# Kernel optimization log

Measured on AMD Instinct MI355X. Metric: run time of the kernel, lower is better.

Reference implementation:

```python
import jax, jax.numpy as jnp
import numpy as np

DIM = 2048
INTER = 1408          # moe_inter_dim per routed expert
N_EXPERTS = 32
TOPK = 6
N_GROUPS = 8
TOPK_GROUPS = 4
ROUTE_SCALE = 2.5
SHARED_INTER = 2816   # n_shared_experts(2) * moe_inter_dim
T = 8192              # tokens (batch*seq flattened)
INIT = 0.02


def setup_inputs() -> dict:
    key = jax.random.key(0)
    k = jax.random.split(key, 8)
    x = jax.random.normal(k[0], (T, DIM), jnp.float32)
    gate_w = jax.random.normal(k[1], (N_EXPERTS, DIM), jnp.float32) * INIT
    # stacked routed-expert weights (torch Linear convention: [out, in])
    w1 = jax.random.normal(k[2], (N_EXPERTS, INTER, DIM), jnp.float32) * INIT
    w2 = jax.random.normal(k[3], (N_EXPERTS, DIM, INTER), jnp.float32) * INIT
    w3 = jax.random.normal(k[4], (N_EXPERTS, INTER, DIM), jnp.float32) * INIT
    # shared experts (single fused MLP, inter = n_shared * moe_inter_dim)
    sw1 = jax.random.normal(k[5], (SHARED_INTER, DIM), jnp.float32) * INIT
    sw2 = jax.random.normal(k[6], (DIM, SHARED_INTER), jnp.float32) * INIT
    sw3 = jax.random.normal(k[7], (SHARED_INTER, DIM), jnp.float32) * INIT
    return {"x": x, "gate_w": gate_w, "w1": w1, "w2": w2, "w3": w3,
            "sw1": sw1, "sw2": sw2, "sw3": sw3}


def _gate(x, gate_w):
    # sigmoid scores, no bias (dim != 7168), group-limited top-k routing
    scores = jax.nn.sigmoid(x @ gate_w.T)                  # (T, E)
    original = scores
    sg = scores.reshape(x.shape[0], N_GROUPS, -1)          # (T, G, E/G)
    group_scores = sg.max(axis=-1)                         # (T, G)  (amax branch)
    _, gidx = jax.lax.top_k(group_scores, TOPK_GROUPS)     # (T, Gk)
    gmask = jnp.zeros((x.shape[0], N_GROUPS), bool).at[
        jnp.arange(x.shape[0])[:, None], gidx].set(True)
    masked = jnp.where(gmask[:, :, None], sg, 0.0).reshape(x.shape[0], -1)
    _, idx = jax.lax.top_k(masked, TOPK)                   # (T, K)
    w = jnp.take_along_axis(original, idx, axis=1)         # gather pre-mask scores
    w = w / w.sum(axis=-1, keepdims=True)                  # sigmoid normalization
    w = w * ROUTE_SCALE
    return w.astype(x.dtype), idx


def reference(x, gate_w, w1, w2, w3, sw1, sw2, sw3):
    weights, idx = _gate(x, gate_w)                        # (T,K), (T,K) int
    # per-token combine weight for each expert: cw[t,e] = sum_k w[t,k]*[idx==e]
    onehot = jax.nn.one_hot(idx, N_EXPERTS, dtype=weights.dtype)  # (T,K,E)
    cw = jnp.einsum('tk,tke->et', weights, onehot)         # (E, T)

    def expert_step(acc, ew):
        W1, W2, W3, cwe = ew                               # cwe: (T,)
        h = jax.nn.silu(x @ W1.T) * (x @ W3.T)             # (T, INTER)
        return acc + cwe[:, None] * (h @ W2.T), None

    y, _ = jax.lax.scan(expert_step, jnp.zeros_like(x), (w1, w2, w3, cw))
    # shared experts MLP (SwiGLU)
    z = (jax.nn.silu(x @ sw1.T) * (x @ sw3.T)) @ sw2.T
    return y + z
```

## Files before the change

### kernel.cpp

```cpp
#include <hip/hip_runtime.h>
#include <hip/hip_bf16.h>
#include <stdint.h>

typedef unsigned short u16;

#define T_TOK 8192
#define DIM 2048
#define INTER 1408
#define NEXP 32
#define TOPK 6
#define SHINTER 2816
#define SLOTS (T_TOK * TOPK)

typedef __attribute__((ext_vector_type(8))) short bf16x8;
typedef __attribute__((ext_vector_type(4))) float f32x4;

__device__ inline u16 f2bf(float f) {
  union { float f; unsigned u; } c; c.f = f;
  unsigned r = (c.u + 0x7FFFu + ((c.u >> 16) & 1u)) >> 16;
  return (u16)r;
}
__device__ inline float bf2f(u16 h) {
  union { unsigned u; float f; } c; c.u = ((unsigned)h) << 16;
  return c.f;
}

__device__ __forceinline__ void gl16(const void* g, void* l) {
  __builtin_amdgcn_global_load_lds(
      (const __attribute__((address_space(1))) void*)g,
      (__attribute__((address_space(3))) void*)l, 16, 0, 0);
}

__global__ __launch_bounds__(256)
void gate_route_k(const float* __restrict__ x, const float* __restrict__ gw,
                  int* __restrict__ tidx, float* __restrict__ tw,
                  int* __restrict__ counts, u16* __restrict__ xb)
{
  int lane = threadIdx.x & 63, w = threadIdx.x >> 6;
  int t = blockIdx.x * 4 + w;
  __shared__ float sc[4][32];
  __shared__ float gm[4][8];
  const float* xr = x + (size_t)t * DIM + lane * 4;
  float4 xv[8];
#pragma unroll
  for (int i = 0; i < 8; i++) xv[i] = *(const float4*)(xr + i * 256);
  u16* xrow = xb + (size_t)t * DIM + lane * 4;
#pragma unroll
  for (int i = 0; i < 8; i++) {
    union { u16 h[4]; uint2 q; } p;
    p.h[0] = f2bf(xv[i].x); p.h[1] = f2bf(xv[i].y);
    p.h[2] = f2bf(xv[i].z); p.h[3] = f2bf(xv[i].w);
    *(uint2*)(xrow + i * 256) = p.q;
  }
  for (int e = 0; e < NEXP; e++) {
    const float* g = gw + (size_t)e * DIM + lane * 4;
    float acc = 0.f;
#pragma unroll
    for (int i = 0; i < 8; i++) {
      float4 gv = *(const float4*)(g + i * 256);
      acc += xv[i].x * gv.x + xv[i].y * gv.y + xv[i].z * gv.z + xv[i].w * gv.w;
    }
#pragma unroll
    for (int off = 32; off > 0; off >>= 1) acc += __shfl_down(acc, off);
    if (lane == 0) sc[w][e] = 1.f / (1.f + __expf(-acc));
  }
  if (lane == 0) {
#pragma unroll
    for (int g = 0; g < 8; g++)
      gm[w][g] = fmaxf(fmaxf(sc[w][g*4+0], sc[w][g*4+1]), fmaxf(sc[w][g*4+2], sc[w][g*4+3]));
    unsigned gsel = 0u;
    for (int it = 0; it < 4; it++) {
      float best = -1.f; int bi = 0;
      for (int g = 0; g < 8; g++)
        if (!((gsel >> g) & 1u) && gm[w][g] > best) { best = gm[w][g]; bi = g; }
      gsel |= 1u << bi;
    }
    unsigned chosen = 0u; float wsum = 0.f;
    int ids[TOPK]; float wv[TOPK];
#pragma unroll
    for (int it = 0; it < TOPK; it++) {
      float best = -1.f; int bi = 0;
      for (int e = 0; e < NEXP; e++)
        if (((gsel >> (e >> 2)) & 1u) && !((chosen >> e) & 1u) && sc[w][e] > best) { best = sc[w][e]; bi = e; }
      chosen |= 1u << bi; ids[it] = bi; wv[it] = best; wsum += best;
    }
    float s = 2.5f / wsum;
#pragma unroll
    for (int k = 0; k < TOPK; k++) {
      tidx[t * TOPK + k] = ids[k];
      tw[t * TOPK + k] = wv[k] * s;
      atomicAdd(&counts[ids[k]], 1);
    }
  }
}

__global__ void zero32(int* p) { if (threadIdx.x < NEXP) p[threadIdx.x] = 0; }

__global__ __launch_bounds__(1024)
void perm_build_k(const int* __restrict__ counts,
                  const int* __restrict__ tidx, const float* __restrict__ tw,
                  int* __restrict__ ptok, float* __restrict__ pw,
                  int* __restrict__ slotof,
                  int4* __restrict__ desc128, int* __restrict__ ntiles)
{
  int e = blockIdx.x;
  int tid = threadIdx.x, lane = tid & 63, w = tid >> 6;
  __shared__ int wsum[16];
  __shared__ int cursor;
  if (w == 0) {
    int c = (lane < NEXP) ? counts[lane] : 0;
    int inc = c;
#pragma unroll
    for (int d = 1; d < 64; d <<= 1) {
      int v = __shfl_up(inc, d);
      if (lane >= d) inc += v;
    }
    int off_e = inc - c;
    if (e == 0) {
      int nt = (c + 127) >> 7;
      int tinc = nt;
#pragma unroll
      for (int d = 1; d < 64; d <<= 1) {
        int v = __shfl_up(tinc, d);
        if (lane >= d) tinc += v;
      }
      int tex = tinc - nt;
      if (lane < NEXP) {
        for (int i = 0; i < nt; i++) {
          int rem = c - i * 128;
          desc128[tex + i] = make_int4(lane, off_e + i * 128, rem < 128 ? rem : 128, 0);
        }
      }
      if (lane == NEXP - 1) ntiles[0] = tinc;
    }
    if (lane == e) cursor = off_e;
  }
  __syncthreads();
  for (int start = 0; start < SLOTS; start += 1024) {
    int i = start + tid;
    int match = (tidx[i] == e) ? 1 : 0;
    unsigned long long b = __ballot(match);
    if (lane == 0) wsum[w] = __popcll(b);
    __syncthreads();
    int base = cursor;
    int waveoff = 0;
    for (int ww = 0; ww < w; ww++) waveoff += wsum[ww];
    int total = 0;
#pragma unroll
    for (int ww = 0; ww < 16; ww++) total += wsum[ww];
    if (match) {
      int before = __popcll(b & ((1ull << lane) - 1ull));
      int slot = base + waveoff + before;
      ptok[slot] = i / TOPK;
      pw[slot] = tw[i];
      slotof[i] = slot;
    }
    __syncthreads();
    if (tid == 0) cursor = base + total;
  }
}

__global__ __launch_bounds__(256)
void cvt3_k(const float* __restrict__ s0, const float* __restrict__ s1,
            const float* __restrict__ s2, u16* __restrict__ d0,
            u16* __restrict__ d1, u16* __restrict__ d2, int n8)
{
  const float* src = (blockIdx.y == 0) ? s0 : (blockIdx.y == 1) ? s1 : s2;
  u16*         dst = (blockIdx.y == 0) ? d0 : (blockIdx.y == 1) ? d1 : d2;
  int stride = gridDim.x * 256;
  for (size_t i = (size_t)blockIdx.x * 256 + threadIdx.x; i < (size_t)n8; i += stride) {
    size_t j = i * 8;
    float4 a = *(const float4*)(src + j);
    float4 b = *(const float4*)(src + j + 4);
    union { u16 h[8]; uint4 u; } p;
    p.h[0] = f2bf(a.x); p.h[1] = f2bf(a.y); p.h[2] = f2bf(a.z); p.h[3] = f2bf(a.w);
    p.h[4] = f2bf(b.x); p.h[5] = f2bf(b.y); p.h[6] = f2bf(b.z); p.h[7] = f2bf(b.w);
    *(uint4*)(dst + j) = p.u;
  }
}


#define UP_RSEG (416 * 11)
#define DN_SSEG (64 * 8)

__global__ __launch_bounds__(256, 2)
void up2m_k(const u16* __restrict__ xb,
            const u16* __restrict__ w1b, const u16* __restrict__ w3b,
            const u16* __restrict__ sw1b, const u16* __restrict__ sw3b,
            const int* __restrict__ ptok,
            const int4* __restrict__ desc, const int* __restrict__ ntiles,
            u16* __restrict__ H, u16* __restrict__ Hs)
{
  int bid = blockIdx.x;
  bool routed = bid < UP_RSEG;
  int slot_base, rows, n0, hld;
  const u16 *B1, *B3;
  u16* out;
  bool gather;
  if (routed) {
    int rt0 = bid % 416, ct = bid / 416;
    int rt = (rt0 & 7) * 52 + (rt0 >> 3);
    if (rt >= ntiles[0]) return;
    int4 d = desc[rt];
    slot_base = d.y; rows = d.z;
    size_t off = (size_t)d.x * (size_t)INTER * DIM;
    B1 = w1b + off; B3 = w3b + off;
    n0 = ct * 128; hld = INTER; out = H; gather = true;
  } else {
    int b2 = bid - UP_RSEG;
    int rt0 = b2 & 63, ct = b2 >> 6;
    int rt = (rt0 & 7) * 8 + (rt0 >> 3);
    slot_base = rt * 128; rows = 128;
    B1 = sw1b; B3 = sw3b;
    n0 = ct * 128; hld = SHINTER; out = Hs; gather = false;
  }
  int tid = threadIdx.x, lane = tid & 63;
  int w = tid >> 6, wr = w >> 1, wc = w & 1;

  __shared__ u16 As[128][64];
  __shared__ u16 Bs1[128][64];
  __shared__ u16 Bs3[128][64];

  int selem = (((lane & 7) ^ (lane >> 3)) * 8);
  const u16 *a_src[4], *b1_src[4], *b3_src[4];
#pragma unroll
  for (int s = 0; s < 4; s++) {
    int r = w * 32 + s * 8 + (lane >> 3);
    int tok;
    if (gather) { int rr = r < rows ? r : rows - 1; tok = ptok[slot_base + rr]; }
    else tok = slot_base + r;
    a_src[s]  = xb + (size_t)tok * DIM + selem;
    b1_src[s] = B1 + (size_t)(n0 + r) * DIM + selem;
    b3_src[s] = B3 + (size_t)(n0 + r) * DIM + selem;
  }

  f32x4 acc1[4][4], acc3[4][4];
#pragma unroll
  for (int m = 0; m < 4; m++)
#pragma unroll
    for (int n = 0; n < 4; n++) { acc1[m][n] = {0.f,0.f,0.f,0.f}; acc3[m][n] = {0.f,0.f,0.f,0.f}; }

  for (int kk = 0; kk < DIM / 64; kk++) {
    __syncthreads();
#pragma unroll
    for (int s = 0; s < 4; s++) {
      gl16(a_src[s]  + kk * 64, &As [w * 32 + s * 8][0]);
      gl16(b1_src[s] + kk * 64, &Bs1[w * 32 + s * 8][0]);
      gl16(b3_src[s] + kk * 64, &Bs3[w * 32 + s * 8][0]);
    }
    __syncthreads();
#pragma unroll
    for (int h = 0; h < 2; h++) {
      bf16x8 af[4], b1f[4], b3f[4];
      int chk = (h * 4 + (lane >> 4)) ^ (lane & 7);
#pragma unroll
      for (int m = 0; m < 4; m++)
        af[m] = *(const bf16x8*)&As[wr * 64 + m * 16 + (lane & 15)][chk * 8];
#pragma unroll
      for (int n = 0; n < 4; n++) {
        b1f[n] = *(const bf16x8*)&Bs1[wc * 64 + n * 16 + (lane & 15)][chk * 8];
        b3f[n] = *(const bf16x8*)&Bs3[wc * 64 + n * 16 + (lane & 15)][chk * 8];
      }
#pragma unroll
      for (int m = 0; m < 4; m++)
#pragma unroll
        for (int n = 0; n < 4; n++) {
          acc1[m][n] = __builtin_amdgcn_mfma_f32_16x16x32_bf16(af[m], b1f[n], acc1[m][n], 0, 0, 0);
          acc3[m][n] = __builtin_amdgcn_mfma_f32_16x16x32_bf16(af[m], b3f[n], acc3[m][n], 0, 0, 0);
        }
    }
  }
#pragma unroll
  for (int m = 0; m < 4; m++) {
#pragma unroll
    for (int r = 0; r < 4; r++) {
      int row_local = wr * 64 + m * 16 + (lane >> 4) * 4 + r;
      if (row_local < rows) {
        size_t rowp = (size_t)(slot_base + row_local) * hld + n0 + wc * 64 + (lane & 15);
#pragma unroll
        for (int n = 0; n < 4; n++) {
          float c1 = acc1[m][n][r], c3 = acc3[m][n][r];
          float hval = (c1 / (1.f + __expf(-c1))) * c3;
          out[rowp + n * 16] = f2bf(hval);
        }
      }
    }
  }
}

template<int KD, bool ROUTED>
__device__ __forceinline__ void down3_body(
    u16 (*As)[64], u16 (*Bs1)[64], u16 (*Bs2)[64],
    const u16* __restrict__ A0, const u16* __restrict__ B,
    int slot_base, int rows, int n0,
    const float* __restrict__ pw,
    u16* __restrict__ slotout, float* __restrict__ yout)
{
  constexpr int KSTEPS = KD / 64;
  int tid = threadIdx.x, lane = tid & 63;
  int w = tid >> 6, wr = w >> 1, wc = w & 1;

  int selem = (((lane & 7) ^ (lane >> 3)) * 8);
  const u16 *a_src[4], *b1_src[4], *b2_src[4];
#pragma unroll
  for (int s = 0; s < 4; s++) {
    int r = w * 32 + s * 8 + (lane >> 3);
    a_src[s]  = A0 + (size_t)(slot_base + r) * KD + selem;
    b1_src[s] = B + (size_t)(n0 + r) * KD + selem;
    b2_src[s] = B + (size_t)(n0 + 128 + r) * KD + selem;
  }

  f32x4 acc[4][8];
#pragma unroll
  for (int m = 0; m < 4; m++)
#pragma unroll
    for (int n = 0; n < 8; n++) acc[m][n] = {0.f, 0.f, 0.f, 0.f};

  for (int kk = 0; kk < KSTEPS; kk++) {
    __syncthreads();
#pragma unroll
    for (int s = 0; s < 4; s++) {
      gl16(a_src[s]  + kk * 64, &As [w * 32 + s * 8][0]);
      gl16(b1_src[s] + kk * 64, &Bs1[w * 32 + s * 8][0]);
      gl16(b2_src[s] + kk * 64, &Bs2[w * 32 + s * 8][0]);
    }
    __syncthreads();
#pragma unroll
    for (int h = 0; h < 2; h++) {
      bf16x8 af[4], bv1[4], bv2[4];
      int chk = (h * 4 + (lane >> 4)) ^ (lane & 7);
#pragma unroll
      for (int m = 0; m < 4; m++)
        af[m] = *(const bf16x8*)&As[wr * 64 + m * 16 + (lane & 15)][chk * 8];
#pragma unroll
      for (int n = 0; n < 4; n++) {
        bv1[n] = *(const bf16x8*)&Bs1[wc * 64 + n * 16 + (lane & 15)][chk * 8];
        bv2[n] = *(const bf16x8*)&Bs2[wc * 64 + n * 16 + (lane & 15)][chk * 8];
      }
#pragma unroll
      for (int m = 0; m < 4; m++)
#pragma unroll
        for (int n = 0; n < 4; n++) {
          acc[m][n]     = __builtin_amdgcn_mfma_f32_16x16x32_bf16(af[m], bv1[n], acc[m][n],     0, 0, 0);
          acc[m][n + 4] = __builtin_amdgcn_mfma_f32_16x16x32_bf16(af[m], bv2[n], acc[m][n + 4], 0, 0, 0);
        }
    }
  }
#pragma unroll
  for (int m = 0; m < 4; m++) {
#pragma unroll
    for (int r = 0; r < 4; r++) {
      int row_local = wr * 64 + m * 16 + (lane >> 4) * 4 + r;
      if (row_local < rows) {
        int slot = slot_base + row_local;
        size_t rp = (size_t)slot * DIM + n0 + wc * 64 + (lane & 15);
        if constexpr (ROUTED) {
          float sw = pw[slot];
#pragma unroll
          for (int n = 0; n < 4; n++) {
            slotout[rp + n * 16]       = f2bf(acc[m][n][r] * sw);
            slotout[rp + 128 + n * 16] = f2bf(acc[m][n + 4][r] * sw);
          }
        } else {
#pragma unroll
          for (int n = 0; n < 4; n++) {
            yout[rp + n * 16]       = acc[m][n][r];
            yout[rp + 128 + n * 16] = acc[m][n + 4][r];
          }
        }
      }
    }
  }
}

__global__ __launch_bounds__(256, 2)
void down3m_k(const u16* __restrict__ H, const u16* __restrict__ Hs,
              const u16* __restrict__ w2b, const u16* __restrict__ sw2b,
              const int4* __restrict__ desc, const int* __restrict__ ntiles,
              const float* __restrict__ pw,
              u16* __restrict__ slotout, float* __restrict__ yout)
{
  __shared__ u16 As[128][64];
  __shared__ u16 Bs1[128][64];
  __shared__ u16 Bs2[128][64];
  int bid = blockIdx.x;
  if (bid >= DN_SSEG) {
    int b2 = bid - DN_SSEG;
    int rt0 = b2 % 416, ct = b2 / 416;
    int rt = (rt0 & 7) * 52 + (rt0 >> 3);
    if (rt >= ntiles[0]) return;
    int4 d = desc[rt];
    down3_body<INTER, true>(As, Bs1, Bs2, H, w2b + (size_t)d.x * DIM * INTER,
                            d.y, d.z, ct * 256, pw, slotout, yout);
  } else {
    int rt0 = bid & 63, ct = bid >> 6;
    int rt = (rt0 & 7) * 8 + (rt0 >> 3);
    down3_body<SHINTER, false>(As, Bs1, Bs2, Hs, sw2b, rt * 128, 128, ct * 256,
                               pw, slotout, yout);
  }
}

template<bool SHARED>
__global__ __launch_bounds__(256, 2)
void up_gemm_k(const u16* __restrict__ xb,
               const float* __restrict__ W1g, const float* __restrict__ W3g,
               const int* __restrict__ ptok,
               const int4* __restrict__ desc, const int* __restrict__ ntiles,
               u16* __restrict__ Hout)
{
  constexpr int HLD = SHARED ? SHINTER : INTER;
  int row_tile = blockIdx.x, col_tile = blockIdx.y;
  int slot_base, rows;
  const float *B1, *B3;
  if constexpr (SHARED) {
    slot_base = row_tile * 128; rows = 128; B1 = W1g; B3 = W3g;
  } else {
    if (row_tile >= ntiles[0]) return;
    int4 d = desc[row_tile];
    slot_base = d.y; rows = d.z;
    size_t off = (size_t)d.x * (size_t)INTER * DIM;
    B1 = W1g + off; B3 = W3g + off;
  }
  int n0 = col_tile * 128;
  int tid = threadIdx.x, lane = tid & 63;
  int wv = tid >> 6, wr = wv >> 1, wc = wv & 1;

  __shared__ u16 As[128][72];
  __shared__ u16 Bs1[128][72];
  __shared__ u16 Bs3[128][72];

  int ar = tid >> 3, ac = (tid & 7) * 8;
  const u16* asrc[4];
#pragma unroll
  for (int s = 0; s < 4; s++) {
    int r = s * 32 + ar;
    int tok;
    if constexpr (SHARED) tok = slot_base + r;
    else { int rr = r < rows ? r : rows - 1; tok = ptok[slot_base + rr]; }
    asrc[s] = xb + (size_t)tok * DIM + ac;
  }
  int br = tid >> 4, bc = (tid & 15) * 4;
  const float* b1p = B1 + (size_t)(n0 + br) * DIM + bc;
  const float* b3p = B3 + (size_t)(n0 + br) * DIM + bc;

  f32x4 acc1[4][4], acc3[4][4];
#pragma unroll
  for (int m = 0; m < 4; m++)
#pragma unroll
    for (int n = 0; n < 4; n++) { acc1[m][n] = {0.f,0.f,0.f,0.f}; acc3[m][n] = {0.f,0.f,0.f,0.f}; }

  for (int kk = 0; kk < DIM / 64; kk++) {
    __syncthreads();
#pragma unroll
    for (int s = 0; s < 4; s++) {
      uint4 v = *(const uint4*)(asrc[s] + kk * 64);
      *(uint4*)&As[s * 32 + ar][ac] = v;
    }
#pragma unroll
    for (int s = 0; s < 8; s++) {
      float4 v = *(const float4*)(b1p + (size_t)(s * 16) * DIM + kk * 64);
      union { u16 h[4]; uint2 q; } o;
      o.h[0] = f2bf(v.x); o.h[1] = f2bf(v.y); o.h[2] = f2bf(v.z); o.h[3] = f2bf(v.w);
      *(uint2*)&Bs1[s * 16 + br][bc] = o.q;
    }
#pragma unroll
    for (int s = 0; s < 8; s++) {
      float4 v = *(const float4*)(b3p + (size_t)(s * 16) * DIM + kk * 64);
      union { u16 h[4]; uint2 q; } o;
      o.h[0] = f2bf(v.x); o.h[1] = f2bf(v.y); o.h[2] = f2bf(v.z); o.h[3] = f2bf(v.w);
      *(uint2*)&Bs3[s * 16 + br][bc] = o.q;
    }
    __syncthreads();
#pragma unroll
    for (int h = 0; h < 2; h++) {
      bf16x8 af[4], b1f[4], b3f[4];
#pragma unroll
      for (int m = 0; m < 4; m++)
        af[m] = *(const bf16x8*)&As[wr * 64 + m * 16 + (lane & 15)][h * 32 + (lane >> 4) * 8];
#pragma unroll
      for (int n = 0; n < 4; n++) {
        b1f[n] = *(const bf16x8*)&Bs1[wc * 64 + n * 16 + (lane & 15)][h * 32 + (lane >> 4) * 8];
        b3f[n] = *(const bf16x8*)&Bs3[wc * 64 + n * 16 + (lane & 15)][h * 32 + (lane >> 4) * 8];
      }
#pragma unroll
      for (int m = 0; m < 4; m++)
#pragma unroll
        for (int n = 0; n < 4; n++) {
          acc1[m][n] = __builtin_amdgcn_mfma_f32_16x16x32_bf16(af[m], b1f[n], acc1[m][n], 0, 0, 0);
          acc3[m][n] = __builtin_amdgcn_mfma_f32_16x16x32_bf16(af[m], b3f[n], acc3[m][n], 0, 0, 0);
        }
    }
  }
#pragma unroll
  for (int m = 0; m < 4; m++) {
#pragma unroll
    for (int r = 0; r < 4; r++) {
      int row_local = wr * 64 + m * 16 + (lane >> 4) * 4 + r;
      if (row_local < rows) {
        size_t rowp = (size_t)(slot_base + row_local) * HLD + n0 + wc * 64 + (lane & 15);
#pragma unroll
        for (int n = 0; n < 4; n++) {
          float c1 = acc1[m][n][r], c3 = acc3[m][n][r];
          float hval = (c1 / (1.f + __expf(-c1))) * c3;
          Hout[rowp + n * 16] = f2bf(hval);
        }
      }
    }
  }
}

template<bool SHARED>
__global__ __launch_bounds__(256, 2)
void down_gemm_k(const u16* __restrict__ Hin, const float* __restrict__ Bg,
                 const int4* __restrict__ desc, const int* __restrict__ ntiles,
                 const float* __restrict__ pw,
                 u16* __restrict__ slotout, float* __restrict__ yout)
{
  constexpr int KD = SHARED ? SHINTER : INTER;
  constexpr int KSTEPS = KD / 64;
  int row_tile = blockIdx.x, col_tile = blockIdx.y;
  int slot_base, rows; const float* B;
  if constexpr (SHARED) { slot_base = row_tile * 128; rows = 128; B = Bg; }
  else {
    if (row_tile >= ntiles[0]) return;
    int4 d = desc[row_tile]; slot_base = d.y; rows = d.z;
    B = Bg + (size_t)d.x * DIM * INTER;
  }
  int n0 = col_tile * 128;
  int tid = threadIdx.x, lane = tid & 63;
  int wv = tid >> 6, wr = wv >> 1, wc = wv & 1;
  __shared__ u16 As[128][72];
  __shared__ u16 Bs[128][72];
  int ar = tid >> 3, ac = (tid & 7) * 8;
  const u16* asrc[4];
#pragma unroll
  for (int s = 0; s < 4; s++)
    asrc[s] = Hin + (size_t)(slot_base + s * 32 + ar) * KD + ac;
  int br = tid >> 4, bc = (tid & 15) * 4;
  const float* bp = B + (size_t)(n0 + br) * KD + bc;

  f32x4 acc[4][4];
#pragma unroll
  for (int m = 0; m < 4; m++)
#pragma unroll
    for (int n = 0; n < 4; n++) acc[m][n] = {0.f,0.f,0.f,0.f};

  for (int kk = 0; kk < KSTEPS; kk++) {
    __syncthreads();
#pragma unroll
    for (int s = 0; s < 4; s++) {
      uint4 v = *(const uint4*)(asrc[s] + kk * 64);
      *(uint4*)&As[s * 32 + ar][ac] = v;
    }
#pragma unroll
    for (int s = 0; s < 8; s++) {
      float4 v = *(const float4*)(bp + (size_t)(s * 16) * KD + kk * 64);
      union { u16 h[4]; uint2 q; } o;
      o.h[0] = f2bf(v.x); o.h[1] = f2bf(v.y); o.h[2] = f2bf(v.z); o.h[3] = f2bf(v.w);
      *(uint2*)&Bs[s * 16 + br][bc] = o.q;
    }
    __syncthreads();
#pragma unroll
    for (int h = 0; h < 2; h++) {
      bf16x8 af[4], bfv[4];
#pragma unroll
      for (int m = 0; m < 4; m++)
        af[m] = *(const bf16x8*)&As[wr * 64 + m * 16 + (lane & 15)][h * 32 + (lane >> 4) * 8];
#pragma unroll
      for (int n = 0; n < 4; n++)
        bfv[n] = *(const bf16x8*)&Bs[wc * 64 + n * 16 + (lane & 15)][h * 32 + (lane >> 4) * 8];
#pragma unroll
      for (int m = 0; m < 4; m++)
#pragma unroll
        for (int n = 0; n < 4; n++)
          acc[m][n] = __builtin_amdgcn_mfma_f32_16x16x32_bf16(af[m], bfv[n], acc[m][n], 0, 0, 0);
    }
  }
#pragma unroll
  for (int m = 0; m < 4; m++) {
#pragma unroll
    for (int r = 0; r < 4; r++) {
      int row_local = wr * 64 + m * 16 + (lane >> 4) * 4 + r;
      if (row_local < rows) {
        int slot = slot_base + row_local;
        size_t rp = (size_t)slot * DIM + n0 + wc * 64 + (lane & 15);
        if constexpr (SHARED) {
#pragma unroll
          for (int n = 0; n < 4; n++) yout[rp + n * 16] = acc[m][n][r];
        } else {
          float sw = pw[slot];
#pragma unroll
          for (int n = 0; n < 4; n++) slotout[rp + n * 16] = f2bf(acc[m][n][r] * sw);
        }
      }
    }
  }
}

__global__ __launch_bounds__(256)
void combine_k(float* __restrict__ y, const u16* __restrict__ slotout, const int* __restrict__ slotof)
{
  int t = blockIdx.x;
  int c = threadIdx.x * 8;
  size_t rp = (size_t)t * DIM + c;
  float4 a = *(const float4*)(y + rp);
  float4 b = *(const float4*)(y + rp + 4);
  float o[8] = {a.x, a.y, a.z, a.w, b.x, b.y, b.z, b.w};
#pragma unroll
  for (int k = 0; k < TOPK; k++) {
    int s = slotof[t * TOPK + k];
    uint4 v = *(const uint4*)(slotout + (size_t)s * DIM + c);
    o[0] += bf2f((u16)(v.x & 0xFFFFu)); o[1] += bf2f((u16)(v.x >> 16));
    o[2] += bf2f((u16)(v.y & 0xFFFFu)); o[3] += bf2f((u16)(v.y >> 16));
    o[4] += bf2f((u16)(v.z & 0xFFFFu)); o[5] += bf2f((u16)(v.z >> 16));
    o[6] += bf2f((u16)(v.w & 0xFFFFu)); o[7] += bf2f((u16)(v.w >> 16));
  }
  *(float4*)(y + rp)     = make_float4(o[0], o[1], o[2], o[3]);
  *(float4*)(y + rp + 4) = make_float4(o[4], o[5], o[6], o[7]);
}

extern "C" void kernel_launch(void* const* d_in, const int* in_sizes, int n_in,
                              void* d_out, int out_size, void* d_ws, size_t ws_size,
                              hipStream_t stream)
{
  const float* x   = (const float*)d_in[0];
  const float* gw  = (const float*)d_in[1];
  const float* w1  = (const float*)d_in[2];
  const float* w2  = (const float*)d_in[3];
  const float* w3  = (const float*)d_in[4];
  const float* sw1 = (const float*)d_in[5];
  const float* sw2 = (const float*)d_in[6];
  const float* sw3 = (const float*)d_in[7];
  float* y = (float*)d_out;
  char* ws = (char*)d_ws;

  int*   counts  = (int*)(ws + 0);
  int*   ntiles  = (int*)(ws + 256);
  int4*  desc128 = (int4*)(ws + 1024);
  int*   tidx    = (int*)(ws + 16384);
  float* tw      = (float*)(ws + 212992);
  int*   ptok    = (int*)(ws + 409600);
  float* pw      = (float*)(ws + 606208);
  int*   slotof  = (int*)(ws + 802816);
  u16*   xb      = (u16*)(ws + 1048576);
  u16*   H       = (u16*)(ws + 34603008ull);
  u16*   Hs      = (u16*)(ws + 173735936ull);
  u16*   sout    = (u16*)(ws + 219873280ull);
  u16*   w1b     = (u16*)(ws + 421199872ull);
  u16*   w3b     = (u16*)(ws + 605749248ull);
  u16*   w2b     = (u16*)(ws + 790298624ull);
  u16*   sw1b    = (u16*)(ws + 974848000ull);
  u16*   sw3b    = (u16*)(ws + 986382336ull);
  u16*   sw2b    = (u16*)(ws + 997916672ull);
  const unsigned long long NEED_FULL = 1009451008ull;

  zero32<<<1, 64, 0, stream>>>(counts);
  gate_route_k<<<2048, 256, 0, stream>>>(x, gw, tidx, tw, counts, xb);
  perm_build_k<<<32, 1024, 0, stream>>>(counts, tidx, tw, ptok, pw, slotof,
                                        desc128, ntiles);

  if (ws_size >= NEED_FULL) {
    const int NW = NEXP * INTER * DIM / 8;
    const int NS = SHINTER * DIM / 8;
    cvt3_k<<<dim3(4096, 3), 256, 0, stream>>>(w1, w3, w2, w1b, w3b, w2b, NW);
    cvt3_k<<<dim3(1024, 3), 256, 0, stream>>>(sw1, sw3, sw2, sw1b, sw3b, sw2b, NS);

    up2m_k<<<UP_RSEG + 64 * 22, 256, 0, stream>>>(xb, w1b, w3b, sw1b, sw3b,
                                                  ptok, desc128, ntiles, H, Hs);
    down3m_k<<<DN_SSEG + 416 * 8, 256, 0, stream>>>(H, Hs, w2b, sw2b,
                                                    desc128, ntiles, pw, sout, y);
  } else {
    up_gemm_k<false><<<dim3(416, 11), 256, 0, stream>>>(xb, w1, w3, ptok, desc128, ntiles, H);
    up_gemm_k<true ><<<dim3(64, 22), 256, 0, stream>>>(xb, sw1, sw3, ptok, desc128, ntiles, Hs);
    down_gemm_k<true ><<<dim3(64, 16), 256, 0, stream>>>(Hs, sw2, desc128, ntiles, pw, sout, y);
    down_gemm_k<false><<<dim3(416, 16), 256, 0, stream>>>(H, w2, desc128, ntiles, pw, sout, y);
  }

  combine_k<<<8192, 256, 0, stream>>>(y, sout, slotof);
}
```

Measured before the change: 2.073 ms.

## Double-buffer down-projection GEMM and shrink its tile to 128 columns

The down-projection kernel now uses a 128x128 output tile with two shared-memory buffers. The next K-slice is prefetched while the current one is multiplied, which leaves one barrier per k-step instead of two. The grid doubles in the column direction to keep the same output coverage. This aims to hide global-load latency and cut accumulator register pressure, at the cost of re-reading the A tile (H) twice as often.

New measurement: 2.203 ms. 1.06x slower.

```diff
diff --git a/kernel.cpp b/kernel.cpp
--- a/kernel.cpp
+++ b/kernel.cpp
@@ -181,7 +181,7 @@
 
 
 #define UP_RSEG (416 * 11)
-#define DN_SSEG (64 * 8)
+#define DN_SSEG (64 * 16)
 
 __global__ __launch_bounds__(256, 2)
 void up2m_k(const u16* __restrict__ xb,
@@ -289,8 +289,8 @@
 }
 
 template<int KD, bool ROUTED>
-__device__ __forceinline__ void down3_body(
-    u16 (*As)[64], u16 (*Bs1)[64], u16 (*Bs2)[64],
+__device__ __forceinline__ void down2p_body(
+    u16 (*As)[128][64], u16 (*Bs)[128][64],
     const u16* __restrict__ A0, const u16* __restrict__ B,
     int slot_base, int rows, int n0,
     const float* __restrict__ pw,
@@ -301,51 +301,55 @@
   int w = tid >> 6, wr = w >> 1, wc = w & 1;
 
   int selem = (((lane & 7) ^ (lane >> 3)) * 8);
-  const u16 *a_src[4], *b1_src[4], *b2_src[4];
+  const u16 *a_src[4], *b_src[4];
 #pragma unroll
   for (int s = 0; s < 4; s++) {
     int r = w * 32 + s * 8 + (lane >> 3);
-    a_src[s]  = A0 + (size_t)(slot_base + r) * KD + selem;
-    b1_src[s] = B + (size_t)(n0 + r) * KD + selem;
-    b2_src[s] = B + (size_t)(n0 + 128 + r) * KD + selem;
-  }
-
-  f32x4 acc[4][8];
+    a_src[s] = A0 + (size_t)(slot_base + r) * KD + selem;
+    b_src[s] = B + (size_t)(n0 + r) * KD + selem;
+  }
+
+  f32x4 acc[4][4];
 #pragma unroll
   for (int m = 0; m < 4; m++)
 #pragma unroll
-    for (int n = 0; n < 8; n++) acc[m][n] = {0.f, 0.f, 0.f, 0.f};
+    for (int n = 0; n < 4; n++) acc[m][n] = {0.f, 0.f, 0.f, 0.f};
+
+#pragma unroll
+  for (int s = 0; s < 4; s++) {
+    gl16(a_src[s], &As[0][w * 32 + s * 8][0]);
+    gl16(b_src[s], &Bs[0][w * 32 + s * 8][0]);
+  }
+  __syncthreads();
 
   for (int kk = 0; kk < KSTEPS; kk++) {
-    __syncthreads();
-#pragma unroll
-    for (int s = 0; s < 4; s++) {
-      gl16(a_src[s]  + kk * 64, &As [w * 32 + s * 8][0]);
-      gl16(b1_src[s] + kk * 64, &Bs1[w * 32 + s * 8][0]);
-      gl16(b2_src[s] + kk * 64, &Bs2[w * 32 + s * 8][0]);
-    }
-    __syncthreads();
+    int cur = kk & 1;
+    if (kk + 1 < KSTEPS) {
+#pragma unroll
+      for (int s = 0; s < 4; s++) {
+        gl16(a_src[s] + (size_t)(kk + 1) * 64, &As[cur ^ 1][w * 32 + s * 8][0]);
+        gl16(b_src[s] + (size_t)(kk + 1) * 64, &Bs[cur ^ 1][w * 32 + s * 8][0]);
+      }
+    }
 #pragma unroll
     for (int h = 0; h < 2; h++) {
-      bf16x8 af[4], bv1[4], bv2[4];
+      bf16x8 af[4], bfv[4];
       int chk = (h * 4 + (lane >> 4)) ^ (lane & 7);
 #pragma unroll
       for (int m = 0; m < 4; m++)
-        af[m] = *(const bf16x8*)&As[wr * 64 + m * 16 + (lane & 15)][chk * 8];
-#pragma unroll
-      for (int n = 0; n < 4; n++) {
-        bv1[n] = *(const bf16x8*)&Bs1[wc * 64 + n * 16 + (lane & 15)][chk * 8];
-        bv2[n] = *(const bf16x8*)&Bs2[wc * 64 + n * 16 + (lane & 15)][chk * 8];
-      }
-#pragma unroll
-      for (int m = 0; m < 4; m++)
-#pragma unroll
-        for (int n = 0; n < 4; n++) {
-          acc[m][n]     = __builtin_amdgcn_mfma_f32_16x16x32_bf16(af[m], bv1[n], acc[m][n],     0, 0, 0);
-          acc[m][n + 4] = __builtin_amdgcn_mfma_f32_16x16x32_bf16(af[m], bv2[n], acc[m][n + 4], 0, 0, 0);
-        }
-    }
-  }
+        af[m] = *(const bf16x8*)&As[cur][wr * 64 + m * 16 + (lane & 15)][chk * 8];
+#pragma unroll
+      for (int n = 0; n < 4; n++)
+        bfv[n] = *(const bf16x8*)&Bs[cur][wc * 64 + n * 16 + (lane & 15)][chk * 8];
+#pragma unroll
+      for (int m = 0; m < 4; m++)
+#pragma unroll
+        for (int n = 0; n < 4; n++)
+          acc[m][n] = __builtin_amdgcn_mfma_f32_16x16x32_bf16(af[m], bfv[n], acc[m][n], 0, 0, 0);
+    }
+    __syncthreads();
+  }
+
 #pragma unroll
   for (int m = 0; m < 4; m++) {
 #pragma unroll
@@ -357,16 +361,10 @@
         if constexpr (ROUTED) {
           float sw = pw[slot];
 #pragma unroll
-          for (int n = 0; n < 4; n++) {
-            slotout[rp + n * 16]       = f2bf(acc[m][n][r] * sw);
-            slotout[rp + 128 + n * 16] = f2bf(acc[m][n + 4][r] * sw);
-          }
+          for (int n = 0; n < 4; n++) slotout[rp + n * 16] = f2bf(acc[m][n][r] * sw);
         } else {
 #pragma unroll
-          for (int n = 0; n < 4; n++) {
-            yout[rp + n * 16]       = acc[m][n][r];
-            yout[rp + 128 + n * 16] = acc[m][n + 4][r];
-          }
+          for (int n = 0; n < 4; n++) yout[rp + n * 16] = acc[m][n][r];
         }
       }
     }
@@ -374,15 +372,14 @@
 }
 
 __global__ __launch_bounds__(256, 2)
-void down3m_k(const u16* __restrict__ H, const u16* __restrict__ Hs,
+void down2p_k(const u16* __restrict__ H, const u16* __restrict__ Hs,
               const u16* __restrict__ w2b, const u16* __restrict__ sw2b,
               const int4* __restrict__ desc, const int* __restrict__ ntiles,
               const float* __restrict__ pw,
               u16* __restrict__ slotout, float* __restrict__ yout)
 {
-  __shared__ u16 As[128][64];
-  __shared__ u16 Bs1[128][64];
-  __shared__ u16 Bs2[128][64];
+  __shared__ u16 As[2][128][64];
+  __shared__ u16 Bs[2][128][64];
   int bid = blockIdx.x;
   if (bid >= DN_SSEG) {
     int b2 = bid - DN_SSEG;
@@ -390,13 +387,13 @@
     int rt = (rt0 & 7) * 52 + (rt0 >> 3);
     if (rt >= ntiles[0]) return;
     int4 d = desc[rt];
-    down3_body<INTER, true>(As, Bs1, Bs2, H, w2b + (size_t)d.x * DIM * INTER,
-                            d.y, d.z, ct * 256, pw, slotout, yout);
+    down2p_body<INTER, true>(As, Bs, H, w2b + (size_t)d.x * DIM * INTER,
+                             d.y, d.z, ct * 128, pw, slotout, yout);
   } else {
     int rt0 = bid & 63, ct = bid >> 6;
     int rt = (rt0 & 7) * 8 + (rt0 >> 3);
-    down3_body<SHINTER, false>(As, Bs1, Bs2, Hs, sw2b, rt * 128, 128, ct * 256,
-                               pw, slotout, yout);
+    down2p_body<SHINTER, false>(As, Bs, Hs, sw2b, rt * 128, 128, ct * 128,
+                                pw, slotout, yout);
   }
 }
 
@@ -667,8 +664,8 @@
 
     up2m_k<<<UP_RSEG + 64 * 22, 256, 0, stream>>>(xb, w1b, w3b, sw1b, sw3b,
                                                   ptok, desc128, ntiles, H, Hs);
-    down3m_k<<<DN_SSEG + 416 * 8, 256, 0, stream>>>(H, Hs, w2b, sw2b,
-                                                    desc128, ntiles, pw, sout, y);
+    down2p_k<<<DN_SSEG + 416 * 16, 256, 0, stream>>>(H, Hs, w2b, sw2b,
+                                                     desc128, ntiles, pw, sout, y);
   } else {
     up_gemm_k<false><<<dim3(416, 11), 256, 0, stream>>>(xb, w1, w3, ptok, desc128, ntiles, H);
     up_gemm_k<true ><<<dim3(64, 22), 256, 0, stream>>>(xb, sw1, sw3, ptok, desc128, ntiles, Hs);
```
